# Kernel optimization log

Measured on AMD Instinct MI355X. Metric: run time of the kernel, lower is better.

## Reference

```python
import jax, jax.numpy as jnp
import numpy as np

N = 100000      # nodes
E = 1600000     # edges (avg degree 16)
IN, HID, EMB1, EMB2, K = 256, 128, 64, 32, 3


def setup_inputs() -> dict:
    key = jax.random.key(0)
    ks = jax.random.split(key, 8)
    x = jax.random.normal(ks[0], (N, IN), jnp.float32)
    edge_index = jax.random.randint(ks[1], (2, E), 0, N)
    init = lambda k, shape, fan: jax.random.normal(k, shape, jnp.float32) * (1.0 / np.sqrt(fan))
    return {
        "x": x,
        "edge_index": edge_index,
        "W_lin1": init(ks[2], (IN, HID), IN),
        "b_lin1": jnp.zeros((HID,), jnp.float32),
        "W_cheb1": init(ks[3], (K, HID, EMB1), HID),
        "b_cheb1": jnp.zeros((EMB1,), jnp.float32),
        "W_cheb2": init(ks[4], (K, EMB1, EMB2), EMB1),
        "b_cheb2": jnp.zeros((EMB2,), jnp.float32),
        "W_lin2": init(ks[5], (EMB2, 2), EMB2),
        "b_lin2": jnp.zeros((2,), jnp.float32),
    }


def cheb_conv(x, src, dst, norm, W, b):
    # PyG ChebConv (sym norm, lambda_max=2): L_hat = -D^{-1/2} A D^{-1/2}
    # T0 = x; T1 = L_hat x; Tk = 2 L_hat T_{k-1} - T_{k-2}; out = sum_k Tk @ W_k + b
    n = x.shape[0]
    prop = lambda h: jax.ops.segment_sum(h[src] * norm[:, None], dst, num_segments=n)
    Tx0 = x
    out = Tx0 @ W[0]
    Tx1 = prop(Tx0)
    out = out + Tx1 @ W[1]
    for k in range(2, W.shape[0]):
        Tx2 = 2.0 * prop(Tx1) - Tx0
        out = out + Tx2 @ W[k]
        Tx0, Tx1 = Tx1, Tx2
    return out + b


def reference(x, edge_index, W_lin1, b_lin1, W_cheb1, b_cheb1, W_cheb2, b_cheb2, W_lin2, b_lin2):
    src, dst = edge_index[0], edge_index[1]
    deg = jax.ops.segment_sum(jnp.ones((src.shape[0],), x.dtype), src, num_segments=x.shape[0])
    dinv = jnp.where(deg > 0, 1.0 / jnp.sqrt(jnp.where(deg > 0, deg, 1.0)), 0.0)
    norm = -dinv[src] * dinv[dst]  # per-edge weight of scaled Laplacian

    h = jax.nn.relu(x @ W_lin1 + b_lin1)                       # dropout = identity (eval)
    h = jax.nn.relu(cheb_conv(h, src, dst, norm, W_cheb1, b_cheb1))
    h = jax.nn.relu(cheb_conv(h, src, dst, norm, W_cheb2, b_cheb2))
    logits = h @ W_lin2 + b_lin2
    return jax.nn.softmax(logits, axis=1)
```

## Files before the change

### kernel.cpp

```cpp
#include <hip/hip_runtime.h>


constexpr int IN_DIM = 256;
constexpr int HID    = 128;
constexpr int EMB1   = 64;
constexpr int EMB2   = 32;

typedef __attribute__((ext_vector_type(8))) short bf16x8;
typedef __attribute__((ext_vector_type(4))) float f32x4;

__device__ __forceinline__ float bf2f(unsigned short u) {
    return __uint_as_float((unsigned)u << 16);
}
__device__ __forceinline__ unsigned short f2bf(float f) {
    unsigned u = __float_as_uint(f);
    u += 0x7fffu + ((u >> 16) & 1u);
    return (unsigned short)(u >> 16);
}


__global__ __launch_bounds__(256) void bucket_hist(const int* __restrict__ dst, int E,
                                                   unsigned* __restrict__ bucket_cnt) {
    __shared__ unsigned h[128];
    for (int i = threadIdx.x; i < 128; i += 256) h[i] = 0;
    __syncthreads();
    int i0 = blockIdx.x * 4096;
#pragma unroll
    for (int j = 0; j < 16; j++) {
        int i = i0 + j * 256 + threadIdx.x;
        if (i < E) atomicAdd(&h[dst[i] >> 10], 1u);
    }
    __syncthreads();
    for (int i = threadIdx.x; i < 128; i += 256)
        if (h[i]) atomicAdd(&bucket_cnt[i * 16], h[i]);
}

__global__ void bucket_scan(const unsigned* __restrict__ bucket_cnt, int nb,
                            unsigned* __restrict__ bucket_base, unsigned* __restrict__ bucket_fill,
                            int* __restrict__ row_ptr, int N, int E) {
    __shared__ unsigned s[128];
    int t = threadIdx.x;
    unsigned v = (t < nb) ? bucket_cnt[t * 16] : 0;
    s[t] = v;
    __syncthreads();
    for (int off = 1; off < 128; off <<= 1) {
        unsigned u = (t >= off) ? s[t - off] : 0;
        __syncthreads();
        s[t] += u;
        __syncthreads();
    }
    if (t < nb) {
        unsigned excl = s[t] - v;
        bucket_base[t] = excl;
        bucket_fill[t * 16] = excl;
    }
    if (t == nb) bucket_base[nb] = (unsigned)E;
    if (t == 0) row_ptr[N] = E;
}

__global__ __launch_bounds__(256) void bucket_scatter(const int* __restrict__ src,
                                                      const int* __restrict__ dst, int E,
                                                      unsigned* __restrict__ bucket_fill,
                                                      unsigned* __restrict__ tmp) {
    __shared__ unsigned h[128];
    __shared__ unsigned base[128];
    for (int i = threadIdx.x; i < 128; i += 256) h[i] = 0;
    __syncthreads();
    int i0 = blockIdx.x * 4096;
    unsigned pk[16], bk[16];
#pragma unroll
    for (int j = 0; j < 16; j++) {
        int i = i0 + j * 256 + threadIdx.x;
        if (i < E) {
            int sv = src[i], dv = dst[i];
            bk[j] = (unsigned)(dv >> 10);
            pk[j] = (unsigned)sv | ((unsigned)(dv & 1023) << 17);
            atomicAdd(&h[bk[j]], 1u);
        } else {
            bk[j] = 0xffffffffu;
        }
    }
    __syncthreads();
    for (int i = threadIdx.x; i < 128; i += 256)
        base[i] = h[i] ? atomicAdd(&bucket_fill[i * 16], h[i]) : 0u;
    __syncthreads();
    for (int i = threadIdx.x; i < 128; i += 256) h[i] = 0;
    __syncthreads();
#pragma unroll
    for (int j = 0; j < 16; j++) {
        if (bk[j] != 0xffffffffu) {
            unsigned r = atomicAdd(&h[bk[j]], 1u);
            tmp[base[bk[j]] + r] = pk[j];
        }
    }
}

__global__ __launch_bounds__(256) void deg_count(const int* __restrict__ src, int E,
                                                 unsigned* __restrict__ partial) {
    __shared__ unsigned h[8192];
    int r = blockIdx.x >> 7, c = blockIdx.x & 127;
    for (int i = threadIdx.x; i < 8192; i += 256) h[i] = 0;
    __syncthreads();
    int lo = r << 14;
    int per = (E + 127) >> 7;
    int b0 = c * per, b1 = min(b0 + per, E);
    for (int i = b0 + threadIdx.x; i < b1; i += 256) {
        int s = src[i] - lo;
        if ((unsigned)s < 16384u)
            atomicAdd(&h[s >> 1], (s & 1) ? 0x10000u : 1u);
    }
    __syncthreads();
    unsigned* out = partial + ((size_t)blockIdx.x << 13);
    for (int i = threadIdx.x; i < 8192; i += 256) out[i] = h[i];
}

__global__ void deg_reduce(const unsigned* __restrict__ partial, float* __restrict__ dinv, int N) {
    int n = blockIdx.x * 256 + threadIdx.x;
    if (n >= N) return;
    int r = n >> 14, word = (n & 16383) >> 1;
    const unsigned* p = partial + (((size_t)r * 128) << 13) + word;
    unsigned d = 0;
#pragma unroll
    for (int c = 0; c < 128; c++) d += p[(size_t)c << 13];
    d = (n & 1) ? (d >> 16) : (d & 0xffffu);
    dinv[n] = d ? rsqrtf((float)d) : 0.f;
}

__global__ __launch_bounds__(512) void bucket_sort(const unsigned* __restrict__ tmp,
                                                   const unsigned* __restrict__ bucket_base,
                                                   const float* __restrict__ dinv,
                                                   int* __restrict__ row_ptr,
                                                   uint2* __restrict__ epack, int N) {
    __shared__ unsigned lcnt[1024];
    __shared__ unsigned lfill[1024];
    __shared__ float    ldinv[1024];
    __shared__ unsigned ssum[512];
    int b = blockIdx.x;
    unsigned beg = bucket_base[b], end = bucket_base[b + 1];
    int node0 = b << 10;
    int t = threadIdx.x;

    lcnt[t] = 0; lcnt[t + 512] = 0;
    ldinv[t]       = (node0 + t < N)       ? dinv[node0 + t]       : 0.f;
    ldinv[t + 512] = (node0 + t + 512 < N) ? dinv[node0 + t + 512] : 0.f;
    __syncthreads();

    for (unsigned i = beg + t; i < end; i += 512)
        atomicAdd(&lcnt[(tmp[i] >> 17) & 1023], 1u);
    __syncthreads();

    unsigned v0 = lcnt[2 * t], v1 = lcnt[2 * t + 1];
    unsigned sp = v0 + v1;
    ssum[t] = sp;
    __syncthreads();
    for (int off = 1; off < 512; off <<= 1) {
        unsigned u = (t >= off) ? ssum[t - off] : 0;
        __syncthreads();
        ssum[t] += u;
        __syncthreads();
    }
    unsigned exclp = ssum[t] - sp;
    unsigned e0 = beg + exclp, e1 = beg + exclp + v0;
    lfill[2 * t] = e0;
    lfill[2 * t + 1] = e1;
    if (node0 + 2 * t < N)     row_ptr[node0 + 2 * t] = (int)e0;
    if (node0 + 2 * t + 1 < N) row_ptr[node0 + 2 * t + 1] = (int)e1;
    __syncthreads();

    for (unsigned i = beg + t; i < end; i += 512) {
        unsigned pkv = tmp[i];
        unsigned sN = pkv & 0x1ffffu;
        unsigned dl = (pkv >> 17) & 1023u;
        unsigned pos = atomicAdd(&lfill[dl], 1u);
        epack[pos] = make_uint2(sN, __float_as_uint(-dinv[sN] * ldinv[dl]));
    }
}


__global__ void weff_pair(const float* __restrict__ W, int H, int Eo, float* __restrict__ out) {
    int i = blockIdx.x * blockDim.x + threadIdx.x;
    if (i >= H * 2 * Eo) return;
    int h = i / (2 * Eo), n = i % (2 * Eo);
    out[i] = (n < Eo) ? W[(size_t)H * Eo + h * Eo + n]
                      : 2.f * W[(size_t)2 * H * Eo + h * Eo + (n - Eo)];
}

__global__ void weff_diff(const float* __restrict__ W, int H, int Eo, float* __restrict__ out) {
    int i = blockIdx.x * blockDim.x + threadIdx.x;
    if (i < H * Eo) out[i] = W[i] - W[(size_t)2 * H * Eo + i];
}


template <int BN, int KTOT, bool AF32, bool HEAD>
__global__ __launch_bounds__(256) void mfma_gemm(
    const void* __restrict__ Av, int Nrows,
    const float* __restrict__ B, const float* __restrict__ bias,
    const unsigned short* __restrict__ Vadd,
    unsigned short* __restrict__ C, int do_relu,
    const float* __restrict__ Whead, const float* __restrict__ bhead,
    float* __restrict__ outp)
{
    constexpr int KSTEPS = KTOT / 32;
    constexpr int NT = BN / 16;

    __shared__ unsigned short Bs[BN][KTOT];
    __shared__ unsigned short As[64][56];

    const int tid = threadIdx.x;
    const int w = tid >> 6;
    const int l = tid & 63;
    const int lr = l & 15;
    const int g  = l >> 4;
    const int row0 = blockIdx.x * 64;

    for (int idx = tid; idx < (KTOT / 2) * BN; idx += 256) {
        int n = idx % BN, k = (idx / BN) * 2;
        float w0 = B[(size_t)k * BN + n];
        float w1 = B[(size_t)(k + 1) * BN + n];
        unsigned pk = (unsigned)f2bf(w0) | ((unsigned)f2bf(w1) << 16);
        int sw = (k >> 3) ^ (n & 7);
        *reinterpret_cast<unsigned*>(&Bs[n][sw * 8 + (k & 7)]) = pk;
    }

    float biasv[NT];
#pragma unroll
    for (int t = 0; t < NT; t++) biasv[t] = bias ? bias[t * 16 + lr] : 0.f;

    f32x4 acc[NT];
#pragma unroll
    for (int t = 0; t < NT; t++) acc[t] = (f32x4){0.f, 0.f, 0.f, 0.f};

    const int arow = tid >> 2;
    const int aq = tid & 3;
    const int grow_a = row0 + arow;
    uint4 areg;

    auto loadA = [&](int ks) {
        int kloc = ks * 32 + aq * 8;
        uint4 v = make_uint4(0u, 0u, 0u, 0u);
        if (grow_a < Nrows) {
            if constexpr (AF32) {
                const float* p = (const float*)Av + (size_t)grow_a * KTOT + kloc;
                float4 a0 = *reinterpret_cast<const float4*>(p);
                float4 a1 = *reinterpret_cast<const float4*>(p + 4);
                v.x = (unsigned)f2bf(a0.x) | ((unsigned)f2bf(a0.y) << 16);
                v.y = (unsigned)f2bf(a0.z) | ((unsigned)f2bf(a0.w) << 16);
                v.z = (unsigned)f2bf(a1.x) | ((unsigned)f2bf(a1.y) << 16);
                v.w = (unsigned)f2bf(a1.z) | ((unsigned)f2bf(a1.w) << 16);
            } else {
                v = *reinterpret_cast<const uint4*>((const unsigned short*)Av +
                                                    (size_t)grow_a * KTOT + kloc);
            }
        }
        areg = v;
    };

    loadA(0);
    __syncthreads();

    for (int ks = 0; ks < KSTEPS; ks++) {
        *reinterpret_cast<uint4*>(&As[arow][aq * 8]) = areg;
        __syncthreads();
        if (ks + 1 < KSTEPS) loadA(ks + 1);

        bf16x8 af = *reinterpret_cast<const bf16x8*>(&As[w * 16 + lr][g * 8]);
#pragma unroll
        for (int t = 0; t < NT; t++) {
            int sw = ((ks * 4 + g) ^ (lr & 7));
            bf16x8 bf = *reinterpret_cast<const bf16x8*>(&Bs[t * 16 + lr][sw * 8]);
            acc[t] = __builtin_amdgcn_mfma_f32_16x16x32_bf16(af, bf, acc[t], 0, 0, 0);
        }
        __syncthreads();
    }

    if constexpr (HEAD) {
        float wc0[NT], wc1[NT];
#pragma unroll
        for (int t = 0; t < NT; t++) {
            wc0[t] = Whead[(t * 16 + lr) * 2 + 0];
            wc1[t] = Whead[(t * 16 + lr) * 2 + 1];
        }
#pragma unroll
        for (int r = 0; r < 4; r++) {
            int grow = row0 + w * 16 + g * 4 + r;
            bool ok = grow < Nrows;
            float p0 = 0.f, p1 = 0.f;
#pragma unroll
            for (int t = 0; t < NT; t++) {
                float v = acc[t][r] + biasv[t];
                if (ok && Vadd) v += bf2f(Vadd[(size_t)grow * BN + t * 16 + lr]);
                if (do_relu) v = fmaxf(v, 0.f);
                p0 += v * wc0[t];
                p1 += v * wc1[t];
            }
#pragma unroll
            for (int off = 8; off >= 1; off >>= 1) {
                p0 += __shfl_xor(p0, off, 16);
                p1 += __shfl_xor(p1, off, 16);
            }
            if (ok && lr == 0) {
                p0 += bhead[0]; p1 += bhead[1];
                float m = fmaxf(p0, p1);
                float e0 = expf(p0 - m), e1 = expf(p1 - m);
                float s = e0 + e1;
                outp[(size_t)grow * 2 + 0] = e0 / s;
                outp[(size_t)grow * 2 + 1] = e1 / s;
            }
        }
    } else {
#pragma unroll
        for (int t = 0; t < NT; t++) {
#pragma unroll
            for (int r = 0; r < 4; r++) {
                int grow = row0 + w * 16 + g * 4 + r;
                if (grow < Nrows) {
                    float v = acc[t][r] + biasv[t];
                    if (Vadd) v += bf2f(Vadd[(size_t)grow * BN + t * 16 + lr]);
                    if (do_relu) v = fmaxf(v, 0.f);
                    C[(size_t)grow * BN + t * 16 + lr] = f2bf(v);
                }
            }
        }
    }
}


template <int F, bool ADD>
__global__ __launch_bounds__(256) void prop_kernel(
    const unsigned short* __restrict__ h, int hstride, int hoff,
    const unsigned short* __restrict__ adds, int astride, int aoff,
    const int* __restrict__ row_ptr, const uint2* __restrict__ epack,
    unsigned short* __restrict__ out, int Nn)
{
    constexpr int LANES = F / 2;
    constexpr int SLOTS = 64 / LANES;
    int node = blockIdx.x * 4 + (threadIdx.x >> 6);
    if (node >= Nn) return;
    int lane = threadIdx.x & 63;
    int fl = (lane % LANES) * 2;
    int slot = lane / LANES;
    int beg = row_ptr[node], end = row_ptr[node + 1];
    const unsigned short* hp = h + hoff + fl;

    float ax = 0.f, ay = 0.f;
    int i = beg + slot;
    for (; i + SLOTS < end; i += 2 * SLOTS) {
        uint2 e0 = epack[i];
        uint2 e1 = epack[i + SLOTS];
        unsigned u0 = *reinterpret_cast<const unsigned*>(&hp[(size_t)e0.x * hstride]);
        unsigned u1 = *reinterpret_cast<const unsigned*>(&hp[(size_t)e1.x * hstride]);
        float w0 = __uint_as_float(e0.y), w1 = __uint_as_float(e1.y);
        ax += __uint_as_float(u0 << 16) * w0 + __uint_as_float(u1 << 16) * w1;
        ay += __uint_as_float(u0 & 0xffff0000u) * w0 + __uint_as_float(u1 & 0xffff0000u) * w1;
    }
    if (i < end) {
        uint2 e0 = epack[i];
        unsigned u0 = *reinterpret_cast<const unsigned*>(&hp[(size_t)e0.x * hstride]);
        float w0 = __uint_as_float(e0.y);
        ax += __uint_as_float(u0 << 16) * w0;
        ay += __uint_as_float(u0 & 0xffff0000u) * w0;
    }
    if (SLOTS >= 4) { ax += __shfl_xor(ax, 16); ay += __shfl_xor(ay, 16); }
    ax += __shfl_xor(ax, 32); ay += __shfl_xor(ay, 32);

    if (lane < LANES) {
        if (ADD) {
            unsigned ua = *reinterpret_cast<const unsigned*>(
                &adds[(size_t)node * astride + aoff + fl]);
            ax += __uint_as_float(ua << 16);
            ay += __uint_as_float(ua & 0xffff0000u);
        }
        unsigned o = (unsigned)f2bf(ax) | ((unsigned)f2bf(ay) << 16);
        *reinterpret_cast<unsigned*>(&out[(size_t)node * F + fl]) = o;
    }
}


extern "C" void kernel_launch(void* const* d_in, const int* in_sizes, int n_in,
                              void* d_out, int out_size, void* d_ws, size_t ws_size,
                              hipStream_t stream) {
    const float* x       = (const float*)d_in[0];
    const int*   eidx    = (const int*)d_in[1];
    const float* W_lin1  = (const float*)d_in[2];
    const float* b_lin1  = (const float*)d_in[3];
    const float* W_cheb1 = (const float*)d_in[4];
    const float* b_cheb1 = (const float*)d_in[5];
    const float* W_cheb2 = (const float*)d_in[6];
    const float* b_cheb2 = (const float*)d_in[7];
    const float* W_lin2  = (const float*)d_in[8];
    const float* b_lin2  = (const float*)d_in[9];
    float* out = (float*)d_out;

    const int N = in_sizes[0] / IN_DIM;
    const int E = in_sizes[1] / 2;
    const int* src = eidx;
    const int* dst = eidx + E;
    const int nb = (N + 1023) >> 10;
    const int R  = (N + 16383) >> 14;

    char* base = (char*)d_ws;
    auto alloc = [&](size_t bytes) -> char* {
        char* p = base;
        base += (bytes + 255) & ~(size_t)255;
        return p;
    };
    unsigned short* h0  = (unsigned short*)alloc((size_t)N * HID * 2);
    unsigned short* Y12 = (unsigned short*)alloc((size_t)N * 2 * EMB1 * 2);
    unsigned short* U1  = (unsigned short*)alloc((size_t)N * EMB1 * 2);
    unsigned short* V1  = (unsigned short*)alloc((size_t)N * EMB1 * 2);
    unsigned short* h1  = (unsigned short*)alloc((size_t)N * EMB1 * 2);
    unsigned short* Z12 = (unsigned short*)alloc((size_t)N * 2 * EMB2 * 2);
    unsigned short* U2  = (unsigned short*)alloc((size_t)N * EMB2 * 2);
    unsigned short* V2  = (unsigned short*)alloc((size_t)N * EMB2 * 2);
    float* dinv  = (float*)alloc((size_t)N * 4);
    uint2* epack = (uint2*)alloc((size_t)E * 8);
    unsigned* tmp     = (unsigned*)alloc((size_t)E * 4);
    unsigned* partial = (unsigned*)alloc((size_t)R * 128 * 8192 * 4);
    int* row_ptr      = (int*)alloc((size_t)(N + 1) * 4);
    unsigned* bucket_cnt  = (unsigned*)alloc(128 * 16 * 4);
    unsigned* bucket_base = (unsigned*)alloc(129 * 4);
    unsigned* bucket_fill = (unsigned*)alloc(128 * 16 * 4);
    float* Wp1 = (float*)alloc((size_t)HID * 2 * EMB1 * 4);
    float* Wd1 = (float*)alloc((size_t)HID * EMB1 * 4);
    float* Wp2 = (float*)alloc((size_t)EMB1 * 2 * EMB2 * 4);
    float* Wd2 = (float*)alloc((size_t)EMB1 * EMB2 * 4);

    hipMemsetAsync(bucket_cnt, 0, 128 * 16 * 4, stream);

    const int EB = (E + 4095) / 4096;
    bucket_hist<<<EB, 256, 0, stream>>>(dst, E, bucket_cnt);
    bucket_scan<<<1, 128, 0, stream>>>(bucket_cnt, nb, bucket_base, bucket_fill, row_ptr, N, E);
    bucket_scatter<<<EB, 256, 0, stream>>>(src, dst, E, bucket_fill, tmp);
    deg_count<<<R * 128, 256, 0, stream>>>(src, E, partial);
    deg_reduce<<<(N + 255) / 256, 256, 0, stream>>>(partial, dinv, N);
    bucket_sort<<<nb, 512, 0, stream>>>(tmp, bucket_base, dinv, row_ptr, epack, N);

    const int tb = 256;
    weff_pair<<<(HID * 2 * EMB1 + tb - 1) / tb, tb, 0, stream>>>(W_cheb1, HID, EMB1, Wp1);
    weff_diff<<<(HID * EMB1 + tb - 1) / tb, tb, 0, stream>>>(W_cheb1, HID, EMB1, Wd1);
    weff_pair<<<(EMB1 * 2 * EMB2 + tb - 1) / tb, tb, 0, stream>>>(W_cheb2, EMB1, EMB2, Wp2);
    weff_diff<<<(EMB1 * EMB2 + tb - 1) / tb, tb, 0, stream>>>(W_cheb2, EMB1, EMB2, Wd2);

    const int ggrid = (N + 63) / 64;
    const int pgrid = (N + 3) / 4;

    mfma_gemm<HID, IN_DIM, true, false><<<ggrid, 256, 0, stream>>>(
        x, N, W_lin1, b_lin1, nullptr, h0, 1, nullptr, nullptr, nullptr);
    mfma_gemm<2 * EMB1, HID, false, false><<<ggrid, 256, 0, stream>>>(
        h0, N, Wp1, nullptr, nullptr, Y12, 0, nullptr, nullptr, nullptr);
    prop_kernel<EMB1, true><<<pgrid, 256, 0, stream>>>(
        Y12, 2 * EMB1, EMB1, Y12, 2 * EMB1, 0, row_ptr, epack, U1, N);
    prop_kernel<EMB1, false><<<pgrid, 256, 0, stream>>>(
        U1, EMB1, 0, nullptr, 0, 0, row_ptr, epack, V1, N);
    mfma_gemm<EMB1, HID, false, false><<<ggrid, 256, 0, stream>>>(
        h0, N, Wd1, b_cheb1, V1, h1, 1, nullptr, nullptr, nullptr);
    mfma_gemm<2 * EMB2, EMB1, false, false><<<ggrid, 256, 0, stream>>>(
        h1, N, Wp2, nullptr, nullptr, Z12, 0, nullptr, nullptr, nullptr);
    prop_kernel<EMB2, true><<<pgrid, 256, 0, stream>>>(
        Z12, 2 * EMB2, EMB2, Z12, 2 * EMB2, 0, row_ptr, epack, U2, N);
    prop_kernel<EMB2, false><<<pgrid, 256, 0, stream>>>(
        U2, EMB2, 0, nullptr, 0, 0, row_ptr, epack, V2, N);
    mfma_gemm<EMB2, EMB1, false, true><<<ggrid, 256, 0, stream>>>(
        h1, N, Wd2, b_cheb2, V2, nullptr, 1, W_lin2, b_lin2, out);
}
```

Measured before the change: 605.7 us.

## Pre-pack weights into MFMA fragment layout and double-buffer A tiles

Adds a bprep kernel that converts each weight matrix once into bf16, pre-arranged in the per-lane MFMA fragment order. The GEMM then reads B fragments straight from global/L2 instead of every block converting and staging the whole weight matrix in LDS. The A tile becomes double-buffered so each k-step needs one barrier instead of two. Separately, the degree-count split is halved (64 column chunks instead of 128), which shrinks the partial buffer and the reduction work. The trade-off is more global B loads per k-step, which now depend on cache hits.

```diff
diff --git a/kernel.cpp b/kernel.cpp
--- a/kernel.cpp
+++ b/kernel.cpp
@@ -98,11 +98,11 @@
 __global__ __launch_bounds__(256) void deg_count(const int* __restrict__ src, int E,
                                                  unsigned* __restrict__ partial) {
     __shared__ unsigned h[8192];
-    int r = blockIdx.x >> 7, c = blockIdx.x & 127;
+    int r = blockIdx.x >> 6, c = blockIdx.x & 63;
     for (int i = threadIdx.x; i < 8192; i += 256) h[i] = 0;
     __syncthreads();
     int lo = r << 14;
-    int per = (E + 127) >> 7;
+    int per = (E + 63) >> 6;
     int b0 = c * per, b1 = min(b0 + per, E);
     for (int i = b0 + threadIdx.x; i < b1; i += 256) {
         int s = src[i] - lo;
@@ -118,10 +118,10 @@
     int n = blockIdx.x * 256 + threadIdx.x;
     if (n >= N) return;
     int r = n >> 14, word = (n & 16383) >> 1;
-    const unsigned* p = partial + (((size_t)r * 128) << 13) + word;
+    const unsigned* p = partial + (((size_t)r * 64) << 13) + word;
     unsigned d = 0;
 #pragma unroll
-    for (int c = 0; c < 128; c++) d += p[(size_t)c << 13];
+    for (int c = 0; c < 64; c++) d += p[(size_t)c << 13];
     d = (n & 1) ? (d >> 16) : (d & 0xffffu);
     dinv[n] = d ? rsqrtf((float)d) : 0.f;
 }
@@ -177,24 +177,28 @@
 }
 
 
-__global__ void weff_pair(const float* __restrict__ W, int H, int Eo, float* __restrict__ out) {
-    int i = blockIdx.x * blockDim.x + threadIdx.x;
-    if (i >= H * 2 * Eo) return;
-    int h = i / (2 * Eo), n = i % (2 * Eo);
-    out[i] = (n < Eo) ? W[(size_t)H * Eo + h * Eo + n]
-                      : 2.f * W[(size_t)2 * H * Eo + h * Eo + (n - Eo)];
-}
-
-__global__ void weff_diff(const float* __restrict__ W, int H, int Eo, float* __restrict__ out) {
-    int i = blockIdx.x * blockDim.x + threadIdx.x;
-    if (i < H * Eo) out[i] = W[i] - W[(size_t)2 * H * Eo + i];
+__global__ void bprep(const float* __restrict__ W, int K, int BN, int Eo, int mode,
+                      unsigned short* __restrict__ out) {
+    int i = blockIdx.x * 256 + threadIdx.x;
+    if (i >= K * BN) return;
+    int j = i & 7, l = (i >> 3) & 63, ft = i >> 9;
+    int NT = BN >> 4;
+    int ks = ft / NT, t = ft - ks * NT;
+    int k = ks * 32 + ((l >> 4) << 3) + j;
+    int n = (t << 4) + (l & 15);
+    float v;
+    if (mode == 0)      v = W[(size_t)k * BN + n];
+    else if (mode == 1) v = (n < Eo) ? W[((size_t)K + k) * Eo + n]
+                                     : 2.f * W[((size_t)2 * K + k) * Eo + (n - Eo)];
+    else                v = W[(size_t)k * Eo + n] - W[((size_t)2 * K + k) * Eo + n];
+    out[i] = f2bf(v);
 }
 
 
 template <int BN, int KTOT, bool AF32, bool HEAD>
 __global__ __launch_bounds__(256) void mfma_gemm(
     const void* __restrict__ Av, int Nrows,
-    const float* __restrict__ B, const float* __restrict__ bias,
+    const unsigned short* __restrict__ Bf, const float* __restrict__ bias,
     const unsigned short* __restrict__ Vadd,
     unsigned short* __restrict__ C, int do_relu,
     const float* __restrict__ Whead, const float* __restrict__ bhead,
@@ -203,8 +207,7 @@
     constexpr int KSTEPS = KTOT / 32;
     constexpr int NT = BN / 16;
 
-    __shared__ unsigned short Bs[BN][KTOT];
-    __shared__ unsigned short As[64][56];
+    __shared__ unsigned short As[2][64][40];
 
     const int tid = threadIdx.x;
     const int w = tid >> 6;
@@ -212,23 +215,6 @@
     const int lr = l & 15;
     const int g  = l >> 4;
     const int row0 = blockIdx.x * 64;
-
-    for (int idx = tid; idx < (KTOT / 2) * BN; idx += 256) {
-        int n = idx % BN, k = (idx / BN) * 2;
-        float w0 = B[(size_t)k * BN + n];
-        float w1 = B[(size_t)(k + 1) * BN + n];
-        unsigned pk = (unsigned)f2bf(w0) | ((unsigned)f2bf(w1) << 16);
-        int sw = (k >> 3) ^ (n & 7);
-        *reinterpret_cast<unsigned*>(&Bs[n][sw * 8 + (k & 7)]) = pk;
-    }
-
-    float biasv[NT];
-#pragma unroll
-    for (int t = 0; t < NT; t++) biasv[t] = bias ? bias[t * 16 + lr] : 0.f;
-
-    f32x4 acc[NT];
-#pragma unroll
-    for (int t = 0; t < NT; t++) acc[t] = (f32x4){0.f, 0.f, 0.f, 0.f};
 
     const int arow = tid >> 2;
     const int aq = tid & 3;
@@ -255,22 +241,32 @@
         areg = v;
     };
 
+    float biasv[NT];
+#pragma unroll
+    for (int t = 0; t < NT; t++) biasv[t] = bias ? bias[t * 16 + lr] : 0.f;
+
+    f32x4 acc[NT];
+#pragma unroll
+    for (int t = 0; t < NT; t++) acc[t] = (f32x4){0.f, 0.f, 0.f, 0.f};
+
     loadA(0);
+    *reinterpret_cast<uint4*>(&As[0][arow][aq * 8]) = areg;
+    if (KSTEPS > 1) loadA(1);
     __syncthreads();
 
     for (int ks = 0; ks < KSTEPS; ks++) {
-        *reinterpret_cast<uint4*>(&As[arow][aq * 8]) = areg;
-        __syncthreads();
-        if (ks + 1 < KSTEPS) loadA(ks + 1);
-
-        bf16x8 af = *reinterpret_cast<const bf16x8*>(&As[w * 16 + lr][g * 8]);
+        bf16x8 af = *reinterpret_cast<const bf16x8*>(&As[ks & 1][w * 16 + lr][g * 8]);
+        if (ks + 1 < KSTEPS) {
+            *reinterpret_cast<uint4*>(&As[(ks + 1) & 1][arow][aq * 8]) = areg;
+            if (ks + 2 < KSTEPS) loadA(ks + 2);
+        }
+        const unsigned short* bp = Bf + ((size_t)(ks * NT) * 64 + l) * 8;
 #pragma unroll
         for (int t = 0; t < NT; t++) {
-            int sw = ((ks * 4 + g) ^ (lr & 7));
-            bf16x8 bf = *reinterpret_cast<const bf16x8*>(&Bs[t * 16 + lr][sw * 8]);
+            bf16x8 bf = *reinterpret_cast<const bf16x8*>(bp + t * 512);
             acc[t] = __builtin_amdgcn_mfma_f32_16x16x32_bf16(af, bf, acc[t], 0, 0, 0);
         }
-        __syncthreads();
+        if (ks + 1 < KSTEPS) __syncthreads();
     }
 
     if constexpr (HEAD) {
@@ -415,15 +411,16 @@
     float* dinv  = (float*)alloc((size_t)N * 4);
     uint2* epack = (uint2*)alloc((size_t)E * 8);
     unsigned* tmp     = (unsigned*)alloc((size_t)E * 4);
-    unsigned* partial = (unsigned*)alloc((size_t)R * 128 * 8192 * 4);
+    unsigned* partial = (unsigned*)alloc((size_t)R * 64 * 8192 * 4);
     int* row_ptr      = (int*)alloc((size_t)(N + 1) * 4);
     unsigned* bucket_cnt  = (unsigned*)alloc(128 * 16 * 4);
     unsigned* bucket_base = (unsigned*)alloc(129 * 4);
     unsigned* bucket_fill = (unsigned*)alloc(128 * 16 * 4);
-    float* Wp1 = (float*)alloc((size_t)HID * 2 * EMB1 * 4);
-    float* Wd1 = (float*)alloc((size_t)HID * EMB1 * 4);
-    float* Wp2 = (float*)alloc((size_t)EMB1 * 2 * EMB2 * 4);
-    float* Wd2 = (float*)alloc((size_t)EMB1 * EMB2 * 4);
+    unsigned short* Bf_l1 = (unsigned short*)alloc((size_t)IN_DIM * HID * 2);
+    unsigned short* Bf_p1 = (unsigned short*)alloc((size_t)HID * 2 * EMB1 * 2);
+    unsigned short* Bf_d1 = (unsigned short*)alloc((size_t)HID * EMB1 * 2);
+    unsigned short* Bf_p2 = (unsigned short*)alloc((size_t)EMB1 * 2 * EMB2 * 2);
+    unsigned short* Bf_d2 = (unsigned short*)alloc((size_t)EMB1 * EMB2 * 2);
 
     hipMemsetAsync(bucket_cnt, 0, 128 * 16 * 4, stream);
 
@@ -431,35 +428,36 @@
     bucket_hist<<<EB, 256, 0, stream>>>(dst, E, bucket_cnt);
     bucket_scan<<<1, 128, 0, stream>>>(bucket_cnt, nb, bucket_base, bucket_fill, row_ptr, N, E);
     bucket_scatter<<<EB, 256, 0, stream>>>(src, dst, E, bucket_fill, tmp);
-    deg_count<<<R * 128, 256, 0, stream>>>(src, E, partial);
+    deg_count<<<R * 64, 256, 0, stream>>>(src, E, partial);
     deg_reduce<<<(N + 255) / 256, 256, 0, stream>>>(partial, dinv, N);
     bucket_sort<<<nb, 512, 0, stream>>>(tmp, bucket_base, dinv, row_ptr, epack, N);
 
     const int tb = 256;
-    weff_pair<<<(HID * 2 * EMB1 + tb - 1) / tb, tb, 0, stream>>>(W_cheb1, HID, EMB1, Wp1);
-    weff_diff<<<(HID * EMB1 + tb - 1) / tb, tb, 0, stream>>>(W_cheb1, HID, EMB1, Wd1);
-    weff_pair<<<(EMB1 * 2 * EMB2 + tb - 1) / tb, tb, 0, stream>>>(W_cheb2, EMB1, EMB2, Wp2);
-    weff_diff<<<(EMB1 * EMB2 + tb - 1) / tb, tb, 0, stream>>>(W_cheb2, EMB1, EMB2, Wd2);
+    bprep<<<(IN_DIM * HID + tb - 1) / tb, tb, 0, stream>>>(W_lin1, IN_DIM, HID, 0, 0, Bf_l1);
+    bprep<<<(HID * 2 * EMB1 + tb - 1) / tb, tb, 0, stream>>>(W_cheb1, HID, 2 * EMB1, EMB1, 1, Bf_p1);
+    bprep<<<(HID * EMB1 + tb - 1) / tb, tb, 0, stream>>>(W_cheb1, HID, EMB1, EMB1, 2, Bf_d1);
+    bprep<<<(EMB1 * 2 * EMB2 + tb - 1) / tb, tb, 0, stream>>>(W_cheb2, EMB1, 2 * EMB2, EMB2, 1, Bf_p2);
+    bprep<<<(EMB1 * EMB2 + tb - 1) / tb, tb, 0, stream>>>(W_cheb2, EMB1, EMB2, EMB2, 2, Bf_d2);
 
     const int ggrid = (N + 63) / 64;
     const int pgrid = (N + 3) / 4;
 
     mfma_gemm<HID, IN_DIM, true, false><<<ggrid, 256, 0, stream>>>(
-        x, N, W_lin1, b_lin1, nullptr, h0, 1, nullptr, nullptr, nullptr);
+        x, N, Bf_l1, b_lin1, nullptr, h0, 1, nullptr, nullptr, nullptr);
     mfma_gemm<2 * EMB1, HID, false, false><<<ggrid, 256, 0, stream>>>(
-        h0, N, Wp1, nullptr, nullptr, Y12, 0, nullptr, nullptr, nullptr);
+        h0, N, Bf_p1, nullptr, nullptr, Y12, 0, nullptr, nullptr, nullptr);
     prop_kernel<EMB1, true><<<pgrid, 256, 0, stream>>>(
         Y12, 2 * EMB1, EMB1, Y12, 2 * EMB1, 0, row_ptr, epack, U1, N);
     prop_kernel<EMB1, false><<<pgrid, 256, 0, stream>>>(
         U1, EMB1, 0, nullptr, 0, 0, row_ptr, epack, V1, N);
     mfma_gemm<EMB1, HID, false, false><<<ggrid, 256, 0, stream>>>(
-        h0, N, Wd1, b_cheb1, V1, h1, 1, nullptr, nullptr, nullptr);
+        h0, N, Bf_d1, b_cheb1, V1, h1, 1, nullptr, nullptr, nullptr);
     mfma_gemm<2 * EMB2, EMB1, false, false><<<ggrid, 256, 0, stream>>>(
-        h1, N, Wp2, nullptr, nullptr, Z12, 0, nullptr, nullptr, nullptr);
+        h1, N, Bf_p2, nullptr, nullptr, Z12, 0, nullptr, nullptr, nullptr);
     prop_kernel<EMB2, true><<<pgrid, 256, 0, stream>>>(
         Z12, 2 * EMB2, EMB2, Z12, 2 * EMB2, 0, row_ptr, epack, U2, N);
     prop_kernel<EMB2, false><<<pgrid, 256, 0, stream>>>(
         U2, EMB2, 0, nullptr, 0, 0, row_ptr, epack, V2, N);
     mfma_gemm<EMB2, EMB1, false, true><<<ggrid, 256, 0, stream>>>(
-        h1, N, Wd2, b_cheb2, V2, nullptr, 1, W_lin2, b_lin2, out);
-}
+        h1, N, Bf_d2, b_cheb2, V2, nullptr, 1, W_lin2, b_lin2, out);
+}
```

Result: faster. 569.5 us (-6.0%).
